# Kernel tuning notes

Measured on AMD Instinct MI355X. Metric: run time of the kernel, lower is better.

Reference implementation:

```python
import jax, jax.numpy as jnp
import numpy as np

B, N, S, HID, HEADS = 64, 256, 16, 32, 8
BN_EPS = 1e-5


def setup_inputs() -> dict:
    key = jax.random.key(0)
    k1, k2, k3, k4 = jax.random.split(key, 4)
    stacks = jax.random.normal(k1, (B, N, N, S), dtype=jnp.float32)
    # True = padded node (row masked out), like the torch code's `mask`
    mask = jax.random.bernoulli(k2, 0.2, (B, N))
    # BatchNorm1d(S) params (train mode -> batch stats; affine params below)
    gamma = jnp.ones((S,), jnp.float32)
    beta = jnp.zeros((S,), jnp.float32)
    # Linear(S -> HID), ReLU, Linear(HID -> HEADS)
    W1 = jax.random.normal(k3, (S, HID), dtype=jnp.float32) * (1.0 / np.sqrt(S))
    b1 = jnp.zeros((HID,), jnp.float32)
    W2 = jax.random.normal(k4, (HID, HEADS), dtype=jnp.float32) * (1.0 / np.sqrt(HID))
    b2 = jnp.zeros((HEADS,), jnp.float32)
    return {"stacks": stacks, "mask": mask, "gamma": gamma, "beta": beta,
            "W1": W1, "b1": b1, "W2": W2, "b2": b2}


def reference(stacks, mask, gamma, beta, W1, b1, W2, b2):
    # stacks: [b, n, n, S]; mask: [b, n] bool, True = padded.
    # Torch: rows stacks[~mask] (shape [K, n, S]) are flattened to [K*n, S],
    # passed through BN(train) + Linear + ReLU + Linear, and scattered back
    # into a zero [b, n, n, heads] tensor. Equivalent dense formulation:
    # compute BN stats as a masked mean/var over valid rows, apply the MLP
    # everywhere, then zero out masked rows.
    valid = ~mask                                   # [b, n]
    w = valid.astype(stacks.dtype)[:, :, None, None]  # [b, n, 1, 1]
    n1 = stacks.shape[2]
    count = jnp.sum(valid.astype(stacks.dtype)) * n1  # K * n valid BN rows
    sx = jnp.sum(stacks * w, axis=(0, 1, 2))        # [S]
    sx2 = jnp.sum((stacks * stacks) * w, axis=(0, 1, 2))
    mean = sx / count
    var = sx2 / count - mean * mean                 # biased var (BN train mode)
    xn = (stacks - mean) * (gamma / jnp.sqrt(var + BN_EPS)) + beta
    h = jax.nn.relu(jnp.einsum('bnms,sh->bnmh', xn, W1) + b1)
    y = jnp.einsum('bnmh,hk->bnmk', h, W2) + b2     # [b, n, n, heads]
    return jnp.where(valid[:, :, None, None], y, jnp.zeros((), y.dtype))
```

## Files before the change

kernel.cpp:

```cpp
#include <hip/hip_runtime.h>
#include <hip/hip_bf16.h>

#define BB 64
#define NN 256
#define SS 16
#define HH 32
#define KK 8
#define NROWPAIRS (BB*NN)
#define STATS_BLOCKS 2048


__global__ void prep_kernel(const void* __restrict__ mask_raw,
                            int* __restrict__ mode_out,
                            int* __restrict__ count_out,
                            unsigned char* __restrict__ valid,
                            float* __restrict__ sx,
                            float* __restrict__ sx2) {
    int tid = threadIdx.x;
    if (tid < 16) { sx[tid] = 0.0f; sx2[tid] = 0.0f; }

    __shared__ int s_flags[2];
    __shared__ int s_mode;
    __shared__ int s_count;
    if (tid < 2) s_flags[tid] = 0;
    if (tid == 0) s_count = 0;
    __syncthreads();

    const unsigned int* w = (const unsigned int*)mask_raw;
    int f_float = 0, f_bool = 0;
    for (int i = tid; i < 4096; i += 1024) {
        unsigned int v = w[i];
        if (v == 0x3F800000u) f_float = 1;
        if (((v >> 8) & 0xFFu) == 1u || ((v >> 16) & 0xFFu) == 1u ||
            ((v >> 24) & 0xFFu) == 1u) f_bool = 1;
    }
    if (f_float) atomicOr(&s_flags[0], 1);
    if (f_bool)  atomicOr(&s_flags[1], 1);
    __syncthreads();
    if (tid == 0) {
        int mode = s_flags[1] ? 1 : (s_flags[0] ? 2 : 0);
        s_mode = mode;
        *mode_out = mode;
    }
    __syncthreads();
    int mode = s_mode;

    int localc = 0;
    for (int i = tid; i < NROWPAIRS; i += 1024) {
        int masked;
        if (mode == 1)      masked = ((const unsigned char*)mask_raw)[i] != 0;
        else if (mode == 2) masked = ((const float*)mask_raw)[i] != 0.0f;
        else                masked = ((const int*)mask_raw)[i] != 0;
        unsigned char v = (unsigned char)(masked ? 0 : 1);
        valid[i] = v;
        localc += v;
    }
    atomicAdd(&s_count, localc);
    __syncthreads();
    if (tid == 0) *count_out = s_count;
}

__global__ __launch_bounds__(256) void stats_kernel(
        const float* __restrict__ stacks,
        const unsigned char* __restrict__ valid,
        float* __restrict__ sx, float* __restrict__ sx2) {
    int tid = threadIdx.x;
    float4 s1 = make_float4(0.f, 0.f, 0.f, 0.f);
    float4 s2 = make_float4(0.f, 0.f, 0.f, 0.f);

    for (int k = 0; k < NROWPAIRS / STATS_BLOCKS; ++k) {
        int chunk = blockIdx.x + k * STATS_BLOCKS;
        if (!valid[chunk]) continue;
        const float4* p = (const float4*)stacks + (size_t)chunk * 1024;
        #pragma unroll
        for (int it = 0; it < 4; ++it) {
            float4 v = p[tid + it * 256];
            s1.x += v.x; s1.y += v.y; s1.z += v.z; s1.w += v.w;
            s2.x += v.x * v.x; s2.y += v.y * v.y;
            s2.z += v.z * v.z; s2.w += v.w * v.w;
        }
    }

    __shared__ float lds[8 * 256];
    lds[0 * 256 + tid] = s1.x; lds[1 * 256 + tid] = s1.y;
    lds[2 * 256 + tid] = s1.z; lds[3 * 256 + tid] = s1.w;
    lds[4 * 256 + tid] = s2.x; lds[5 * 256 + tid] = s2.y;
    lds[6 * 256 + tid] = s2.z; lds[7 * 256 + tid] = s2.w;
    __syncthreads();

    if (tid < 32) {
        int kind = tid >> 4;
        int s = tid & 15;
        int g = s >> 2, c = (s & 3) + kind * 4;
        float tot = 0.f;
        for (int i = 0; i < 64; ++i) tot += lds[c * 256 + (g + i * 4)];
        atomicAdd(kind ? &sx2[s] : &sx[s], tot);
    }
}

__global__ void weights_kernel(const float* __restrict__ gamma,
                               const float* __restrict__ beta,
                               const float* __restrict__ W1,
                               const float* __restrict__ b1,
                               const float* __restrict__ sx,
                               const float* __restrict__ sx2,
                               const int* __restrict__ count_rows,
                               float* __restrict__ W1c,
                               float* __restrict__ b1c) {
    __shared__ float s_scale[SS], s_shift[SS];
    int tid = threadIdx.x;
    if (tid < SS) {
        float cnt = (float)(*count_rows) * (float)NN;
        if (cnt < 1.0f) cnt = 1.0f;
        float mean = sx[tid] / cnt;
        float var  = sx2[tid] / cnt - mean * mean;
        float sc   = gamma[tid] / sqrtf(var + 1e-5f);
        s_scale[tid] = sc;
        s_shift[tid] = beta[tid] - mean * sc;
    }
    __syncthreads();
    if (tid < SS * HH) W1c[tid] = s_scale[tid >> 5] * W1[tid];
    if (tid < HH) {
        float acc = b1[tid];
        #pragma unroll
        for (int s = 0; s < SS; ++s) acc += s_shift[s] * W1[s * HH + tid];
        b1c[tid] = acc;
    }
}

__global__ __launch_bounds__(256) void mlp_kernel(
        const float* __restrict__ stacks,
        const unsigned char* __restrict__ valid,
        const float* __restrict__ W1c,
        const float* __restrict__ b1c,
        const float* __restrict__ W2,
        const float* __restrict__ b2,
        float* __restrict__ out) {
    int bid = blockIdx.x;
    int tid = threadIdx.x;
    size_t row = (size_t)bid * NN + tid;
    float4* outp = (float4*)out + row * 2;

    if (!valid[bid]) {
        float4 z = make_float4(0.f, 0.f, 0.f, 0.f);
        outp[0] = z; outp[1] = z;
        return;
    }

    const float4* xp = (const float4*)stacks + row * 4;
    float4 x0 = xp[0], x1 = xp[1], x2 = xp[2], x3 = xp[3];
    float x[SS] = { x0.x, x0.y, x0.z, x0.w,  x1.x, x1.y, x1.z, x1.w,
                    x2.x, x2.y, x2.z, x2.w,  x3.x, x3.y, x3.z, x3.w };

    float h[HH];
    #pragma unroll
    for (int j = 0; j < HH; ++j) h[j] = b1c[j];
    #pragma unroll
    for (int k = 0; k < SS; ++k) {
        float xk = x[k];
        #pragma unroll
        for (int j = 0; j < HH; ++j) h[j] = fmaf(xk, W1c[k * HH + j], h[j]);
    }
    #pragma unroll
    for (int j = 0; j < HH; ++j) h[j] = fmaxf(h[j], 0.0f);

    float y[KK];
    #pragma unroll
    for (int i = 0; i < KK; ++i) y[i] = b2[i];
    #pragma unroll
    for (int j = 0; j < HH; ++j) {
        float hj = h[j];
        #pragma unroll
        for (int i = 0; i < KK; ++i) y[i] = fmaf(hj, W2[j * KK + i], y[i]);
    }

    outp[0] = make_float4(y[0], y[1], y[2], y[3]);
    outp[1] = make_float4(y[4], y[5], y[6], y[7]);
}

extern "C" void kernel_launch(void* const* d_in, const int* in_sizes, int n_in,
                              void* d_out, int out_size, void* d_ws, size_t ws_size,
                              hipStream_t stream) {
    const float* stacks = (const float*)d_in[0];
    const void*  mask   = d_in[1];
    const float* gamma  = (const float*)d_in[2];
    const float* beta   = (const float*)d_in[3];
    const float* W1     = (const float*)d_in[4];
    const float* b1     = (const float*)d_in[5];
    const float* W2     = (const float*)d_in[6];
    const float* b2     = (const float*)d_in[7];
    float* out = (float*)d_out;

    char* ws = (char*)d_ws;
    int*           mode      = (int*)(ws + 0);
    int*           countRows = (int*)(ws + 4);
    unsigned char* valid     = (unsigned char*)(ws + 64);
    float*         sx        = (float*)(ws + 16448);
    float*         sx2       = (float*)(ws + 16512);
    float*         b1c       = (float*)(ws + 16576);
    float*         W1c       = (float*)(ws + 16704);

    prep_kernel<<<1, 1024, 0, stream>>>(mask, mode, countRows, valid, sx, sx2);
    stats_kernel<<<STATS_BLOCKS, 256, 0, stream>>>(stacks, valid, sx, sx2);
    weights_kernel<<<1, 512, 0, stream>>>(gamma, beta, W1, b1, sx, sx2,
                                          countRows, W1c, b1c);
    mlp_kernel<<<NROWPAIRS, 256, 0, stream>>>(stacks, valid, W1c, b1c, W2, b2, out);
}
```

Before: 485.2 us.

## Fuse mask prep into stats kernel and replace atomics with per-block partials

The single-block prep kernel is removed. Each stats block now detects the mask dtype itself and computes validity for its own 8 row chunks. Instead of float atomics into global sums, each block writes per-block partial sums and counts, and the weights kernel reduces them with an LDS tree. This drops one serial launch and global atomic contention, at the cost of every block redundantly re-reading 16KB of mask for dtype detection.

```diff
diff --git a/kernel.cpp b/kernel.cpp
--- a/kernel.cpp
+++ b/kernel.cpp
@@ -1,34 +1,33 @@
 #include <hip/hip_runtime.h>
-#include <hip/hip_bf16.h>
-
-#define BB 64
+
 #define NN 256
 #define SS 16
 #define HH 32
 #define KK 8
-#define NROWPAIRS (BB*NN)
+#define NROWPAIRS 16384
 #define STATS_BLOCKS 2048
 
 
-__global__ void prep_kernel(const void* __restrict__ mask_raw,
-                            int* __restrict__ mode_out,
-                            int* __restrict__ count_out,
-                            unsigned char* __restrict__ valid,
-                            float* __restrict__ sx,
-                            float* __restrict__ sx2) {
+__global__ __launch_bounds__(256) void stats_kernel(
+        const void* __restrict__ mask_raw,
+        const float* __restrict__ stacks,
+        unsigned char* __restrict__ valid,
+        int* __restrict__ count_partial,
+        float* __restrict__ partials) {
     int tid = threadIdx.x;
-    if (tid < 16) { sx[tid] = 0.0f; sx2[tid] = 0.0f; }
+    int bid = blockIdx.x;
 
     __shared__ int s_flags[2];
     __shared__ int s_mode;
     __shared__ int s_count;
+    __shared__ unsigned char s_valid[8];
     if (tid < 2) s_flags[tid] = 0;
     if (tid == 0) s_count = 0;
     __syncthreads();
 
     const unsigned int* w = (const unsigned int*)mask_raw;
     int f_float = 0, f_bool = 0;
-    for (int i = tid; i < 4096; i += 1024) {
+    for (int i = tid; i < 4096; i += 256) {
         unsigned int v = w[i];
         if (v == 0x3F800000u) f_float = 1;
         if (((v >> 8) & 0xFFu) == 1u || ((v >> 16) & 0xFFu) == 1u ||
@@ -37,40 +36,28 @@
     if (f_float) atomicOr(&s_flags[0], 1);
     if (f_bool)  atomicOr(&s_flags[1], 1);
     __syncthreads();
-    if (tid == 0) {
-        int mode = s_flags[1] ? 1 : (s_flags[0] ? 2 : 0);
-        s_mode = mode;
-        *mode_out = mode;
-    }
+    if (tid == 0) s_mode = s_flags[1] ? 1 : (s_flags[0] ? 2 : 0);
     __syncthreads();
     int mode = s_mode;
 
-    int localc = 0;
-    for (int i = tid; i < NROWPAIRS; i += 1024) {
+    if (tid < 8) {
+        int chunk = bid + tid * STATS_BLOCKS;
         int masked;
-        if (mode == 1)      masked = ((const unsigned char*)mask_raw)[i] != 0;
-        else if (mode == 2) masked = ((const float*)mask_raw)[i] != 0.0f;
-        else                masked = ((const int*)mask_raw)[i] != 0;
+        if (mode == 1)      masked = ((const unsigned char*)mask_raw)[chunk] != 0;
+        else if (mode == 2) masked = ((const float*)mask_raw)[chunk] != 0.0f;
+        else                masked = ((const int*)mask_raw)[chunk] != 0;
         unsigned char v = (unsigned char)(masked ? 0 : 1);
-        valid[i] = v;
-        localc += v;
-    }
-    atomicAdd(&s_count, localc);
-    __syncthreads();
-    if (tid == 0) *count_out = s_count;
-}
-
-__global__ __launch_bounds__(256) void stats_kernel(
-        const float* __restrict__ stacks,
-        const unsigned char* __restrict__ valid,
-        float* __restrict__ sx, float* __restrict__ sx2) {
-    int tid = threadIdx.x;
+        s_valid[tid] = v;
+        valid[chunk] = v;
+        if (v) atomicAdd(&s_count, 1);
+    }
+    __syncthreads();
+
     float4 s1 = make_float4(0.f, 0.f, 0.f, 0.f);
     float4 s2 = make_float4(0.f, 0.f, 0.f, 0.f);
-
-    for (int k = 0; k < NROWPAIRS / STATS_BLOCKS; ++k) {
-        int chunk = blockIdx.x + k * STATS_BLOCKS;
-        if (!valid[chunk]) continue;
+    for (int k = 0; k < 8; ++k) {
+        if (!s_valid[k]) continue;
+        int chunk = bid + k * STATS_BLOCKS;
         const float4* p = (const float4*)stacks + (size_t)chunk * 1024;
         #pragma unroll
         for (int it = 0; it < 4; ++it) {
@@ -94,32 +81,57 @@
         int g = s >> 2, c = (s & 3) + kind * 4;
         float tot = 0.f;
         for (int i = 0; i < 64; ++i) tot += lds[c * 256 + (g + i * 4)];
-        atomicAdd(kind ? &sx2[s] : &sx[s], tot);
-    }
-}
-
-__global__ void weights_kernel(const float* __restrict__ gamma,
-                               const float* __restrict__ beta,
-                               const float* __restrict__ W1,
-                               const float* __restrict__ b1,
-                               const float* __restrict__ sx,
-                               const float* __restrict__ sx2,
-                               const int* __restrict__ count_rows,
-                               float* __restrict__ W1c,
-                               float* __restrict__ b1c) {
+        partials[bid * 32 + tid] = tot;
+    }
+    if (tid == 0) count_partial[bid] = s_count;
+}
+
+__global__ __launch_bounds__(512) void weights_kernel(
+        const float* __restrict__ gamma,
+        const float* __restrict__ beta,
+        const float* __restrict__ W1,
+        const float* __restrict__ b1,
+        const float* __restrict__ partials,
+        const int* __restrict__ count_partial,
+        float* __restrict__ W1c,
+        float* __restrict__ b1c) {
+    int tid = threadIdx.x;
+    __shared__ float red[512];
+    __shared__ int s_cnt;
     __shared__ float s_scale[SS], s_shift[SS];
-    int tid = threadIdx.x;
+
+    if (tid == 0) s_cnt = 0;
+
+    {
+        int c = tid & 31, j = tid >> 5;
+        float acc = 0.f;
+        for (int k = j; k < STATS_BLOCKS; k += 16) acc += partials[k * 32 + c];
+        red[tid] = acc;
+    }
+    int cacc = 0;
+    for (int k = tid; k < STATS_BLOCKS; k += 512) cacc += count_partial[k];
+    __syncthreads();
+    if (tid < 256) red[tid] += red[tid + 256];
+    if (cacc) atomicAdd(&s_cnt, cacc);
+    __syncthreads();
+    if (tid < 128) red[tid] += red[tid + 128];
+    __syncthreads();
+    if (tid < 64) red[tid] += red[tid + 64];
+    __syncthreads();
+    if (tid < 32) red[tid] += red[tid + 32];
+    __syncthreads();
+
     if (tid < SS) {
-        float cnt = (float)(*count_rows) * (float)NN;
+        float cnt = (float)s_cnt * (float)NN;
         if (cnt < 1.0f) cnt = 1.0f;
-        float mean = sx[tid] / cnt;
-        float var  = sx2[tid] / cnt - mean * mean;
+        float mean = red[tid] / cnt;
+        float var  = red[16 + tid] / cnt - mean * mean;
         float sc   = gamma[tid] / sqrtf(var + 1e-5f);
         s_scale[tid] = sc;
         s_shift[tid] = beta[tid] - mean * sc;
     }
     __syncthreads();
-    if (tid < SS * HH) W1c[tid] = s_scale[tid >> 5] * W1[tid];
+    W1c[tid] = s_scale[tid >> 5] * W1[tid];
     if (tid < HH) {
         float acc = b1[tid];
         #pragma unroll
@@ -192,17 +204,16 @@
     float* out = (float*)d_out;
 
     char* ws = (char*)d_ws;
-    int*           mode      = (int*)(ws + 0);
-    int*           countRows = (int*)(ws + 4);
-    unsigned char* valid     = (unsigned char*)(ws + 64);
-    float*         sx        = (float*)(ws + 16448);
-    float*         sx2       = (float*)(ws + 16512);
-    float*         b1c       = (float*)(ws + 16576);
-    float*         W1c       = (float*)(ws + 16704);
-
-    prep_kernel<<<1, 1024, 0, stream>>>(mask, mode, countRows, valid, sx, sx2);
-    stats_kernel<<<STATS_BLOCKS, 256, 0, stream>>>(stacks, valid, sx, sx2);
-    weights_kernel<<<1, 512, 0, stream>>>(gamma, beta, W1, b1, sx, sx2,
-                                          countRows, W1c, b1c);
-    mlp_kernel<<<NROWPAIRS, 256, 0, stream>>>(stacks, valid, W1c, b1c, W2, b2, out);
-}
+    unsigned char* valid        = (unsigned char*)(ws + 64);
+    int*           countPartial = (int*)(ws + 16448);
+    float*         partials     = (float*)(ws + 24704);
+    float*         W1c          = (float*)(ws + 286848);
+    float*         b1c          = (float*)(ws + 288896);
+
+    stats_kernel<<<STATS_BLOCKS, 256, 0, stream>>>(mask, stacks, valid,
+                                                   countPartial, partials);
+    weights_kernel<<<1, 512, 0, stream>>>(gamma, beta, W1, b1,
+                                          partials, countPartial, W1c, b1c);
+    mlp_kernel<<<NROWPAIRS, 256, 0, stream>>>(stacks, valid, W1c, b1c,
+                                              W2, b2, out);
+}
```

Result: slower. 496.0 us (+2.2%).
